# Kernel tuning notes

Measured on AMD Instinct MI355X. Metric: run time of the kernel, lower is better.

The kernel has to match this reference:

```python
import jax, jax.numpy as jnp
import numpy as np

B, C, L, H = 4, 512, 2048, 8
DH = C // H
SCALE = DH ** -0.5
EPS = 1e-5  # torch LayerNorm default


def setup_inputs() -> dict:
    key = jax.random.key(0)
    ks = jax.random.split(key, 3)
    x = jax.random.normal(ks[0], (B, C, L), dtype=jnp.float32)
    # Conv1d kernel_size=1 == per-position linear; weights ~ N(0, 1/C)
    w_qkv = jax.random.normal(ks[1], (3 * C, C), dtype=jnp.float32) / np.sqrt(C)
    b_qkv = jnp.zeros((3 * C,), dtype=jnp.float32)
    # NOTE: original uses zero_module(proj_out); random weights used here so the
    # baseline is non-trivial for kernel correctness testing.
    w_proj = jax.random.normal(ks[2], (C, C), dtype=jnp.float32) / np.sqrt(C)
    b_proj = jnp.zeros((C,), dtype=jnp.float32)
    ln_gamma = jnp.ones((C,), dtype=jnp.float32)
    ln_beta = jnp.zeros((C,), dtype=jnp.float32)
    return {"x": x, "ln_gamma": ln_gamma, "ln_beta": ln_beta,
            "w_qkv": w_qkv, "b_qkv": b_qkv, "w_proj": w_proj, "b_proj": b_proj}


def reference(x, ln_gamma, ln_beta, w_qkv, b_qkv, w_proj, b_proj):
    # ChannelNorm: LayerNorm over channel dim. Work in [B, L, C] layout.
    h = jnp.swapaxes(x, 1, 2)                      # [B, L, C]
    mu = jnp.mean(h, axis=-1, keepdims=True)
    var = jnp.mean((h - mu) ** 2, axis=-1, keepdims=True)
    hn = (h - mu) * jax.lax.rsqrt(var + EPS) * ln_gamma + ln_beta

    # QKV 1x1 conv as GEMM: [B, L, 3C]
    qkv = jnp.einsum('blc,dc->bld', hn, w_qkv) + b_qkv
    qkv = qkv.reshape(B, L, 3, H, DH)
    q, k, v = (qkv[:, :, i].transpose(0, 2, 1, 3) for i in range(3))  # [B, H, L, DH]

    # Scaled dot-product attention (full O(L^2) scores, as in source)
    w = jnp.einsum('bhqd,bhkd->bhqk', q, k) * SCALE
    w = jax.nn.softmax(w, axis=-1)
    o = jnp.einsum('bhqk,bhkd->bhqd', w, v)        # [B, H, L, DH]
    o = o.transpose(0, 2, 1, 3).reshape(B, L, C)

    # proj_out 1x1 conv + residual (dropout in eval mode = identity)
    out = jnp.einsum('blc,dc->bld', o, w_proj) + b_proj
    return jnp.swapaxes(out, 1, 2) + x             # [B, C, L]
```

## Files before the change

kernel.cpp:

```cpp
#include <hip/hip_runtime.h>
#include <hip/hip_bf16.h>

typedef __bf16 bf16;
typedef bf16 bf16x8 __attribute__((ext_vector_type(8)));
typedef bf16 bf16x4 __attribute__((ext_vector_type(4)));
typedef float f32x4 __attribute__((ext_vector_type(4)));

constexpr int B = 4, C = 512, L = 2048, H = 8, DH = 64;
constexpr int BL = B * L;
constexpr int BH = B * H;
constexpr int N_QKV = 3 * C;
constexpr float QSCALE = 0.125f * 1.44269504088896f;
constexpr float EPS = 1e-5f;

constexpr size_t SZ = (size_t)BL * C;
constexpr size_t OFF_HN    = 0;
constexpr size_t OFF_WQKV  = OFF_HN    + SZ * 2;
constexpr size_t OFF_WPROJ = OFF_WQKV  + (size_t)N_QKV * C * 2;
constexpr size_t OFF_Q     = OFF_WPROJ + (size_t)C * C * 2;
constexpr size_t OFF_K     = OFF_Q     + SZ * 2;
constexpr size_t OFF_V     = OFF_K     + SZ * 2;
constexpr size_t OFF_O     = OFF_V     + SZ * 2;
constexpr size_t OFF_STATS = OFF_O     + SZ * 2;
constexpr size_t OFF_OPART = OFF_STATS + (size_t)BL * 2 * 4;
constexpr size_t OFF_ML    = OFF_OPART + (size_t)2 * BH * L * DH * 2;

__device__ __forceinline__ bf16x8 ld8(const bf16* p) {
  return *(const bf16x8*)p;
}

__device__ __forceinline__ void gll16(const bf16* g, bf16* l) {
  __builtin_amdgcn_global_load_lds(
      (const __attribute__((address_space(1))) unsigned int*)(const void*)g,
      (__attribute__((address_space(3))) unsigned int*)(void*)l, 16, 0, 0);
}

__device__ __forceinline__ unsigned pack_bf16(float a, float b) {
  unsigned ua = __builtin_bit_cast(unsigned, a) + 0x8000u;
  unsigned ub = __builtin_bit_cast(unsigned, b) + 0x8000u;
  return __builtin_amdgcn_perm(ub, ua, 0x07060302u);
}
__device__ __forceinline__ float bf_lo(unsigned u) { return __builtin_bit_cast(float, u << 16); }
__device__ __forceinline__ float bf_hi(unsigned u) { return __builtin_bit_cast(float, u & 0xFFFF0000u); }

__global__ __launch_bounds__(256) void k_convert_w(const float* __restrict__ wqkv,
                                                   const float* __restrict__ wproj,
                                                   bf16* __restrict__ wqkv_b,
                                                   bf16* __restrict__ wproj_b) {
  int i = blockIdx.x * 256 + threadIdx.x;
  if (i < N_QKV * C) wqkv_b[i] = (bf16)wqkv[i];
  if (i < C * C)     wproj_b[i] = (bf16)wproj[i];
}

__global__ __launch_bounds__(1024) void k_ln_stats(const float* __restrict__ x,
                                                   float* __restrict__ stats) {
  int blk = blockIdx.x;
  int b = blk >> 5;
  int l0 = (blk & 31) << 6;
  int lane = threadIdx.x & 63;
  int w = threadIdx.x >> 6;
  const float* xp = x + ((size_t)b * C) * L + l0 + lane;
  float s = 0.f, ss = 0.f;
#pragma unroll
  for (int r = 0; r < 32; ++r) {
    float v = xp[(size_t)(w + r * 16) * L];
    s += v; ss += v * v;
  }
  __shared__ float sh_s[16][64];
  __shared__ float sh_q[16][64];
  sh_s[w][lane] = s; sh_q[w][lane] = ss;
  __syncthreads();
  if (threadIdx.x < 64) {
    float ts = 0.f, tq = 0.f;
#pragma unroll
    for (int i = 0; i < 16; ++i) { ts += sh_s[i][lane]; tq += sh_q[i][lane]; }
    float mu = ts * (1.0f / C);
    float var = tq * (1.0f / C) - mu * mu;
    float rstd = rsqrtf(var + EPS);
    int idx = b * L + l0 + lane;
    stats[idx * 2]     = mu;
    stats[idx * 2 + 1] = rstd;
  }
}

__global__ __launch_bounds__(256) void k_ln_norm(const float* __restrict__ x,
                                                 const float* __restrict__ stats,
                                                 const float* __restrict__ gamma,
                                                 const float* __restrict__ beta,
                                                 bf16* __restrict__ hn) {
  int blk = blockIdx.x;
  int ct = blk & 7;  blk >>= 3;
  int lt = blk & 31; int b = blk >> 5;
  int c0 = ct << 6, l0 = lt << 6;
  int lane = threadIdx.x & 63, w = threadIdx.x >> 6;
  __shared__ float tile[64][65];
  const float* xp = x + (size_t)(b * C + c0) * L + l0;
#pragma unroll
  for (int r = 0; r < 16; ++r) {
    int c = w * 16 + r;
    tile[c][lane] = xp[(size_t)c * L + lane];
  }
  __syncthreads();
  float g = gamma[c0 + lane], be = beta[c0 + lane];
  bf16* hp = hn + (size_t)(b * L + l0) * C + c0 + lane;
#pragma unroll
  for (int r = 0; r < 16; ++r) {
    int ll = w * 16 + r;
    float mu   = stats[(b * L + l0 + ll) * 2];
    float rstd = stats[(b * L + l0 + ll) * 2 + 1];
    float v = (tile[lane][ll] - mu) * rstd * g + be;
    hp[(size_t)ll * C] = (bf16)v;
  }
}

__global__ __launch_bounds__(256) void k_gemm_qkv(const bf16* __restrict__ hn,
                                                  const bf16* __restrict__ wq,
                                                  const float* __restrict__ bq,
                                                  bf16* __restrict__ qg,
                                                  bf16* __restrict__ kg,
                                                  bf16* __restrict__ vg) {
  int mt = blockIdx.x, nt = blockIdx.y;
  int m0 = mt << 7, n0 = nt << 7;
  int t = threadIdx.x, lane = t & 63, w = t >> 6;
  int mw = w >> 1, nw = w & 1;
  int q4 = lane >> 4, c16 = lane & 15;
  __shared__ __align__(16) char smem[36864];
  bf16* As = (bf16*)smem;
  bf16* Bs = (bf16*)(smem + 16384);

  int goff[4], ldsoff[4];
#pragma unroll
  for (int p = 0; p < 4; ++p) {
    int idx = (p * 4 + w) * 64 + lane;
    int row = idx >> 3, s0 = idx & 7;
    goff[p] = row * C + (s0 ^ (row & 7)) * 8;
    ldsoff[p] = (p * 4 + w) * 512;
  }

  f32x4 acc[4][4];
#pragma unroll
  for (int mi = 0; mi < 4; ++mi)
#pragma unroll
    for (int ni = 0; ni < 4; ++ni) acc[mi][ni] = (f32x4){0.f, 0.f, 0.f, 0.f};

  const bf16* ap = hn + (size_t)m0 * C;
  const bf16* bp = wq + (size_t)n0 * C;
  for (int k0 = 0; k0 < C; k0 += 64) {
    __syncthreads();
#pragma unroll
    for (int p = 0; p < 4; ++p) {
      gll16(ap + k0 + goff[p], As + ldsoff[p]);
      gll16(bp + k0 + goff[p], Bs + ldsoff[p]);
    }
    __syncthreads();
#pragma unroll
    for (int kk2 = 0; kk2 < 2; ++kk2) {
      bf16x8 af[4], bfr[4];
#pragma unroll
      for (int mi = 0; mi < 4; ++mi) {
        int row = mw * 64 + mi * 16 + c16;
        af[mi] = ld8(As + row * 64 + ((kk2 * 4 + q4) ^ (row & 7)) * 8);
      }
#pragma unroll
      for (int ni = 0; ni < 4; ++ni) {
        int row = nw * 64 + ni * 16 + c16;
        bfr[ni] = ld8(Bs + row * 64 + ((kk2 * 4 + q4) ^ (row & 7)) * 8);
      }
#pragma unroll
      for (int mi = 0; mi < 4; ++mi)
#pragma unroll
        for (int ni = 0; ni < 4; ++ni)
          acc[mi][ni] = __builtin_amdgcn_mfma_f32_16x16x32_bf16(af[mi], bfr[ni], acc[mi][ni], 0, 0, 0);
    }
  }
  __syncthreads();

  int i = nt >> 2;
  int h = ((nt & 3) << 1) + nw;
  int b = m0 >> 11;
  int l0 = (m0 & (L - 1)) + mw * 64;
  float bias[4];
#pragma unroll
  for (int ni = 0; ni < 4; ++ni) bias[ni] = bq[n0 + nw * 64 + ni * 16 + c16];
  bf16* Os = (bf16*)(smem + w * 9216);

  if (i == 2) {
#pragma unroll
    for (int mi = 0; mi < 4; ++mi)
#pragma unroll
      for (int ni = 0; ni < 4; ++ni) {
        bf16x4 pk;
#pragma unroll
        for (int r = 0; r < 4; ++r) pk[r] = (bf16)(acc[mi][ni][r] + bias[ni]);
        *(bf16x4*)&Os[(ni * 16 + c16) * 72 + mi * 16 + q4 * 4] = pk;
      }
    __syncthreads();
    const bf16* src = Os + lane * 72;
    bf16* dst = vg + ((size_t)((b * H + h) * DH + lane)) * L + l0;
#pragma unroll
    for (int s = 0; s < 8; ++s)
      *(uint4*)(dst + s * 8) = *(const uint4*)(src + s * 8);
  } else {
    float sc = (i == 0) ? QSCALE : 1.0f;
#pragma unroll
    for (int mi = 0; mi < 4; ++mi)
#pragma unroll
      for (int ni = 0; ni < 4; ++ni)
#pragma unroll
        for (int r = 0; r < 4; ++r)
          Os[(mi * 16 + q4 * 4 + r) * 72 + ni * 16 + c16] = (bf16)((acc[mi][ni][r] + bias[ni]) * sc);
    __syncthreads();
    bf16* dst0 = (i == 0) ? qg : kg;
    const bf16* src = Os + lane * 72;
    bf16* dst = dst0 + ((size_t)((b * H + h) * L + l0 + lane)) * DH;
#pragma unroll
    for (int s = 0; s < 8; ++s)
      *(uint4*)(dst + s * 8) = *(const uint4*)(src + s * 8);
  }
}

__global__ __launch_bounds__(128, 4) void k_attn(const bf16* __restrict__ qg,
                                                 const bf16* __restrict__ kg,
                                                 const bf16* __restrict__ vt,
                                                 bf16* __restrict__ opart,
                                                 float* __restrict__ lsum) {
  int blk = blockIdx.x;
  int js = blk & 1; blk >>= 1;
  int qt = blk & 31; int bh = blk >> 5;
  int t = threadIdx.x, lane = t & 63, w = t >> 6;
  int q4 = lane >> 4, c16 = lane & 15;
  __shared__ __align__(16) bf16 Ks[64][64];
  __shared__ __align__(16) bf16 Vts[64][64];
  __shared__ __align__(16) bf16 Ps[2][16][72];
  const bf16* qptr  = qg + ((size_t)bh * L + qt * 64 + w * 32) * DH;
  const bf16* kptr  = kg + (size_t)bh * L * DH;
  const bf16* vtptr = vt + (size_t)bh * DH * L;

  int ksoff[4], vsoff[4];
#pragma unroll
  for (int p = 0; p < 4; ++p) {
    int idx = (p * 2 + w) * 64 + lane;
    int r = idx >> 3, s0 = idx & 7;
    int ch = s0 ^ (r & 7);
    ksoff[p] = r * DH + ch * 8;
    vsoff[p] = r * L + ch * 8;
  }
  int sw = c16 & 7;

  bf16x8 qf[2][2];
#pragma unroll
  for (int qb = 0; qb < 2; ++qb)
#pragma unroll
    for (int kk2 = 0; kk2 < 2; ++kk2)
      qf[qb][kk2] = ld8(&qptr[(size_t)(qb * 16 + c16) * DH + kk2 * 32 + q4 * 8]);

  f32x4 o_acc[2][4];
  float l_i[2] = {0.f, 0.f};
#pragma unroll
  for (int qb = 0; qb < 2; ++qb)
#pragma unroll
    for (int db = 0; db < 4; ++db) o_acc[qb][db] = (f32x4){0.f, 0.f, 0.f, 0.f};

  for (int j0 = js * 1024; j0 < js * 1024 + 1024; j0 += 64) {
    __syncthreads();
#pragma unroll
    for (int p = 0; p < 4; ++p) {
      gll16(kptr + (size_t)j0 * DH + ksoff[p], &Ks[0][0]  + (p * 2 + w) * 512);
      gll16(vtptr + j0 + vsoff[p],             &Vts[0][0] + (p * 2 + w) * 512);
    }
    __syncthreads();

    f32x4 s[2][4];
#pragma unroll
    for (int qb = 0; qb < 2; ++qb)
#pragma unroll
      for (int jb = 0; jb < 4; ++jb) s[qb][jb] = (f32x4){0.f, 0.f, 0.f, 0.f};
#pragma unroll
    for (int kk2 = 0; kk2 < 2; ++kk2) {
      int choff = ((kk2 * 4 + q4) ^ sw) * 8;
#pragma unroll
      for (int jb = 0; jb < 4; ++jb) {
        bf16x8 kf = ld8(&Ks[0][0] + (jb * 16 + c16) * 64 + choff);
        s[0][jb] = __builtin_amdgcn_mfma_f32_16x16x32_bf16(kf, qf[0][kk2], s[0][jb], 0, 0, 0);
        s[1][jb] = __builtin_amdgcn_mfma_f32_16x16x32_bf16(kf, qf[1][kk2], s[1][jb], 0, 0, 0);
      }
    }

#pragma unroll
    for (int qb = 0; qb < 2; ++qb) {
      float rs = 0.f;
#pragma unroll
      for (int jb = 0; jb < 4; ++jb)
#pragma unroll
        for (int r = 0; r < 4; ++r) {
          float p_ = __builtin_amdgcn_exp2f(s[qb][jb][r]);
          s[qb][jb][r] = p_;
          rs += p_;
        }
      l_i[qb] += rs;
    }

    bf16x8 vf[2][4];
#pragma unroll
    for (int kk2 = 0; kk2 < 2; ++kk2) {
      int choff = ((kk2 * 4 + q4) ^ sw) * 8;
#pragma unroll
      for (int db = 0; db < 4; ++db)
        vf[kk2][db] = ld8(&Vts[0][0] + (db * 16 + c16) * 64 + choff);
    }

#pragma unroll
    for (int qb = 0; qb < 2; ++qb) {
#pragma unroll
      for (int jb = 0; jb < 4; ++jb) {
        uint2 pk;
        pk.x = pack_bf16(s[qb][jb][0], s[qb][jb][1]);
        pk.y = pack_bf16(s[qb][jb][2], s[qb][jb][3]);
        *(uint2*)&Ps[w][c16][jb * 16 + q4 * 4] = pk;
      }
#pragma unroll
      for (int kk2 = 0; kk2 < 2; ++kk2) {
        bf16x8 pf = ld8(&Ps[w][c16][kk2 * 32 + q4 * 8]);
#pragma unroll
        for (int db = 0; db < 4; ++db)
          o_acc[qb][db] = __builtin_amdgcn_mfma_f32_16x16x32_bf16(vf[kk2][db], pf, o_acc[qb][db], 0, 0, 0);
      }
    }
  }

#pragma unroll
  for (int qb = 0; qb < 2; ++qb) {
    float lf = l_i[qb];
    lf += __shfl_xor(lf, 16, 64);
    lf += __shfl_xor(lf, 32, 64);
    int q = qt * 64 + w * 32 + qb * 16 + c16;
    bf16* op = opart + (((size_t)js * BH + bh) * L + q) * DH;
#pragma unroll
    for (int db = 0; db < 4; ++db) {
      uint2 pk;
      pk.x = pack_bf16(o_acc[qb][db][0], o_acc[qb][db][1]);
      pk.y = pack_bf16(o_acc[qb][db][2], o_acc[qb][db][3]);
      *(uint2*)&op[db * 16 + q4 * 4] = pk;
    }
    if (q4 == 0) lsum[((size_t)js * BH + bh) * L + q] = lf;
  }
}

__global__ __launch_bounds__(256) void k_merge(const bf16* __restrict__ opart,
                                               const float* __restrict__ lsum,
                                               bf16* __restrict__ ob) {
  int blk = blockIdx.x;
  int qt = blk & 31, bh = blk >> 5;
  int t = threadIdx.x;
  int q = qt * 64 + (t >> 2);
  int seg = t & 3;
  float l0 = lsum[(size_t)bh * L + q];
  float l1 = lsum[((size_t)BH + bh) * L + q];
  float inv = __builtin_amdgcn_rcpf(l0 + l1);
  const uint4* p0 = (const uint4*)(opart + ((size_t)bh * L + q) * DH + seg * 16);
  const uint4* p1 = (const uint4*)(opart + (((size_t)BH + bh) * L + q) * DH + seg * 16);
  int b = bh >> 3, h = bh & 7;
  uint4* dst = (uint4*)(ob + ((size_t)b * L + q) * C + h * DH + seg * 16);
#pragma unroll
  for (int i = 0; i < 2; ++i) {
    uint4 a0 = p0[i], a1 = p1[i];
    uint4 o;
    unsigned* pa0 = (unsigned*)&a0;
    unsigned* pa1 = (unsigned*)&a1;
    unsigned* po  = (unsigned*)&o;
#pragma unroll
    for (int k = 0; k < 4; ++k) {
      float lo = (bf_lo(pa0[k]) + bf_lo(pa1[k])) * inv;
      float hi = (bf_hi(pa0[k]) + bf_hi(pa1[k])) * inv;
      po[k] = pack_bf16(lo, hi);
    }
    dst[i] = o;
  }
}

__global__ __launch_bounds__(256) void k_gemm_proj(const bf16* __restrict__ ob,
                                                   const bf16* __restrict__ wp,
                                                   const float* __restrict__ bp,
                                                   const float* __restrict__ x,
                                                   float* __restrict__ out) {
  int mt = blockIdx.x, nt = blockIdx.y;
  int m0 = mt << 6, n0 = nt << 6;
  int t = threadIdx.x;
  int lane = t & 63, w = t >> 6;
  int q4 = lane >> 4, c16 = lane & 15;
  __shared__ __align__(16) bf16 As[64][72];
  __shared__ __align__(16) bf16 Bs[64][72];
  __shared__ float Ot[64][65];
  f32x4 acc[4];
#pragma unroll
  for (int nb = 0; nb < 4; ++nb) acc[nb] = (f32x4){0.f, 0.f, 0.f, 0.f};

  for (int k0 = 0; k0 < C; k0 += 64) {
    __syncthreads();
#pragma unroll
    for (int p = 0; p < 2; ++p) {
      int idx = p * 256 + t;
      int row = idx >> 3, ch = idx & 7;
      *(bf16x8*)&As[row][ch * 8] = *(const bf16x8*)&ob[(size_t)(m0 + row) * C + k0 + ch * 8];
      *(bf16x8*)&Bs[row][ch * 8] = *(const bf16x8*)&wp[(size_t)(n0 + row) * C + k0 + ch * 8];
    }
    __syncthreads();
#pragma unroll
    for (int kk = 0; kk < 64; kk += 32) {
      bf16x8 a = ld8(&As[w * 16 + c16][kk + q4 * 8]);
#pragma unroll
      for (int nb = 0; nb < 4; ++nb) {
        bf16x8 bfr = ld8(&Bs[nb * 16 + c16][kk + q4 * 8]);
        acc[nb] = __builtin_amdgcn_mfma_f32_16x16x32_bf16(a, bfr, acc[nb], 0, 0, 0);
      }
    }
  }
  __syncthreads();
#pragma unroll
  for (int nb = 0; nb < 4; ++nb)
#pragma unroll
    for (int r = 0; r < 4; ++r)
      Ot[w * 16 + q4 * 4 + r][nb * 16 + c16] = acc[nb][r];
  __syncthreads();
  int b = m0 >> 11, l0 = m0 & (L - 1);
#pragma unroll
  for (int r = 0; r < 16; ++r) {
    int cl = w * 16 + r;
    int c = n0 + cl;
    size_t idx = (size_t)(b * C + c) * L + l0 + lane;
    out[idx] = Ot[lane][cl] + bp[c] + x[idx];
  }
}

extern "C" void kernel_launch(void* const* d_in, const int* in_sizes, int n_in,
                              void* d_out, int out_size, void* d_ws, size_t ws_size,
                              hipStream_t stream) {
  const float* x     = (const float*)d_in[0];
  const float* gamma = (const float*)d_in[1];
  const float* beta  = (const float*)d_in[2];
  const float* wqkv  = (const float*)d_in[3];
  const float* bqkv  = (const float*)d_in[4];
  const float* wproj = (const float*)d_in[5];
  const float* bproj = (const float*)d_in[6];
  float* out = (float*)d_out;
  char* ws = (char*)d_ws;
  bf16* hn  = (bf16*)(ws + OFF_HN);
  bf16* wqb = (bf16*)(ws + OFF_WQKV);
  bf16* wpb = (bf16*)(ws + OFF_WPROJ);
  bf16* qbp = (bf16*)(ws + OFF_Q);
  bf16* kbp = (bf16*)(ws + OFF_K);
  bf16* vbp = (bf16*)(ws + OFF_V);
  bf16* obp = (bf16*)(ws + OFF_O);
  float* stats = (float*)(ws + OFF_STATS);
  bf16* opart = (bf16*)(ws + OFF_OPART);
  float* lsum = (float*)(ws + OFF_ML);

  hipLaunchKernelGGL(k_convert_w, dim3((N_QKV * C + 255) / 256), dim3(256), 0, stream,
                     wqkv, wproj, wqb, wpb);
  hipLaunchKernelGGL(k_ln_stats, dim3(B * (L / 64)), dim3(1024), 0, stream, x, stats);
  hipLaunchKernelGGL(k_ln_norm, dim3(B * (L / 64) * (C / 64)), dim3(256), 0, stream,
                     x, stats, gamma, beta, hn);
  hipLaunchKernelGGL(k_gemm_qkv, dim3(BL / 128, N_QKV / 128), dim3(256), 0, stream,
                     hn, wqb, bqkv, qbp, kbp, vbp);
  hipLaunchKernelGGL(k_attn, dim3(B * H * (L / 64) * 2), dim3(128), 0, stream,
                     qbp, kbp, vbp, opart, lsum);
  hipLaunchKernelGGL(k_merge, dim3(BH * (L / 64)), dim3(256), 0, stream, opart, lsum, obp);
  hipLaunchKernelGGL(k_gemm_proj, dim3(BL / 64, C / 64), dim3(256), 0, stream,
                     obp, wpb, bproj, x, out);
}
```

Baseline: 202.0 us.

## Fuse LayerNorm passes, fold split-K merge into proj GEMM, widen attention blocks

Merges the two LayerNorm kernels into one that keeps a 512x32 tile of x in LDS, so x is read once and the stats buffer round trip goes away. Removes the separate merge kernel: the projection GEMM now reads both attention partial outputs, combines them and normalises by the summed row sums while staging its A tile. Attention blocks grow to 256 threads covering 128 queries, so each K/V tile load is shared by twice as many queries. The costs are a large LDS footprint in the LN kernel, which limits occupancy, and the merge arithmetic being repeated by every N-tile of the proj GEMM.

```diff
diff --git a/kernel.cpp b/kernel.cpp
--- a/kernel.cpp
+++ b/kernel.cpp
@@ -52,64 +52,52 @@
   if (i < C * C)     wproj_b[i] = (bf16)wproj[i];
 }
 
-__global__ __launch_bounds__(1024) void k_ln_stats(const float* __restrict__ x,
-                                                   float* __restrict__ stats) {
+__global__ __launch_bounds__(1024) void k_ln(const float* __restrict__ x,
+                                             const float* __restrict__ gamma,
+                                             const float* __restrict__ beta,
+                                             bf16* __restrict__ hn) {
   int blk = blockIdx.x;
-  int b = blk >> 5;
-  int l0 = (blk & 31) << 6;
-  int lane = threadIdx.x & 63;
-  int w = threadIdx.x >> 6;
-  const float* xp = x + ((size_t)b * C) * L + l0 + lane;
+  int b = blk >> 6;
+  int l0 = (blk & 63) << 5;
+  int t = threadIdx.x;
+  int ll = t & 31;
+  int cg = t >> 5;
+  __shared__ float tile[512][33];
+  __shared__ float sh_s[32][33];
+  __shared__ float sh_q[32][33];
+  __shared__ float mu_s[32], rs_s[32];
+  const float* xp = x + ((size_t)b * C) * L + l0;
   float s = 0.f, ss = 0.f;
 #pragma unroll
-  for (int r = 0; r < 32; ++r) {
-    float v = xp[(size_t)(w + r * 16) * L];
+  for (int r = 0; r < 16; ++r) {
+    int c = cg * 16 + r;
+    float v = xp[(size_t)c * L + ll];
+    tile[c][ll] = v;
     s += v; ss += v * v;
   }
-  __shared__ float sh_s[16][64];
-  __shared__ float sh_q[16][64];
-  sh_s[w][lane] = s; sh_q[w][lane] = ss;
+  sh_s[cg][ll] = s; sh_q[cg][ll] = ss;
   __syncthreads();
-  if (threadIdx.x < 64) {
+  if (t < 32) {
     float ts = 0.f, tq = 0.f;
 #pragma unroll
-    for (int i = 0; i < 16; ++i) { ts += sh_s[i][lane]; tq += sh_q[i][lane]; }
+    for (int i = 0; i < 32; ++i) { ts += sh_s[i][t]; tq += sh_q[i][t]; }
     float mu = ts * (1.0f / C);
     float var = tq * (1.0f / C) - mu * mu;
-    float rstd = rsqrtf(var + EPS);
-    int idx = b * L + l0 + lane;
-    stats[idx * 2]     = mu;
-    stats[idx * 2 + 1] = rstd;
-  }
-}
-
-__global__ __launch_bounds__(256) void k_ln_norm(const float* __restrict__ x,
-                                                 const float* __restrict__ stats,
-                                                 const float* __restrict__ gamma,
-                                                 const float* __restrict__ beta,
-                                                 bf16* __restrict__ hn) {
-  int blk = blockIdx.x;
-  int ct = blk & 7;  blk >>= 3;
-  int lt = blk & 31; int b = blk >> 5;
-  int c0 = ct << 6, l0 = lt << 6;
-  int lane = threadIdx.x & 63, w = threadIdx.x >> 6;
-  __shared__ float tile[64][65];
-  const float* xp = x + (size_t)(b * C + c0) * L + l0;
-#pragma unroll
-  for (int r = 0; r < 16; ++r) {
-    int c = w * 16 + r;
-    tile[c][lane] = xp[(size_t)c * L + lane];
+    mu_s[t] = mu;
+    rs_s[t] = rsqrtf(var + EPS);
   }
   __syncthreads();
-  float g = gamma[c0 + lane], be = beta[c0 + lane];
-  bf16* hp = hn + (size_t)(b * L + l0) * C + c0 + lane;
-#pragma unroll
-  for (int r = 0; r < 16; ++r) {
-    int ll = w * 16 + r;
-    float mu   = stats[(b * L + l0 + ll) * 2];
-    float rstd = stats[(b * L + l0 + ll) * 2 + 1];
-    float v = (tile[lane][ll] - mu) * rstd * g + be;
-    hp[(size_t)ll * C] = (bf16)v;
+  int c2 = (t & 255) * 2;
+  int lgrp = t >> 8;
+  float g0 = gamma[c2], g1 = gamma[c2 + 1];
+  float b0 = beta[c2],  b1 = beta[c2 + 1];
+#pragma unroll
+  for (int it = 0; it < 8; ++it) {
+    int l = lgrp * 8 + it;
+    float mu = mu_s[l], rstd = rs_s[l];
+    float v0 = (tile[c2][l]     - mu) * rstd * g0 + b0;
+    float v1 = (tile[c2 + 1][l] - mu) * rstd * g1 + b1;
+    *(unsigned*)&hn[(size_t)(b * L + l0 + l) * C + c2] = pack_bf16(v0, v1);
   }
 }
 
@@ -219,31 +207,31 @@
   }
 }
 
-__global__ __launch_bounds__(128, 4) void k_attn(const bf16* __restrict__ qg,
+__global__ __launch_bounds__(256, 4) void k_attn(const bf16* __restrict__ qg,
                                                  const bf16* __restrict__ kg,
                                                  const bf16* __restrict__ vt,
                                                  bf16* __restrict__ opart,
                                                  float* __restrict__ lsum) {
   int blk = blockIdx.x;
   int js = blk & 1; blk >>= 1;
-  int qt = blk & 31; int bh = blk >> 5;
+  int qt = blk & 15; int bh = blk >> 4;
   int t = threadIdx.x, lane = t & 63, w = t >> 6;
   int q4 = lane >> 4, c16 = lane & 15;
   __shared__ __align__(16) bf16 Ks[64][64];
   __shared__ __align__(16) bf16 Vts[64][64];
-  __shared__ __align__(16) bf16 Ps[2][16][72];
-  const bf16* qptr  = qg + ((size_t)bh * L + qt * 64 + w * 32) * DH;
+  __shared__ __align__(16) bf16 Ps[4][16][72];
+  const bf16* qptr  = qg + ((size_t)bh * L + qt * 128 + w * 32) * DH;
   const bf16* kptr  = kg + (size_t)bh * L * DH;
   const bf16* vtptr = vt + (size_t)bh * DH * L;
 
-  int ksoff[4], vsoff[4];
-#pragma unroll
-  for (int p = 0; p < 4; ++p) {
-    int idx = (p * 2 + w) * 64 + lane;
-    int r = idx >> 3, s0 = idx & 7;
-    int ch = s0 ^ (r & 7);
-    ksoff[p] = r * DH + ch * 8;
-    vsoff[p] = r * L + ch * 8;
+  int ksoff[2], vsoff[2];
+#pragma unroll
+  for (int p = 0; p < 2; ++p) {
+    int ci = p * 256 + w * 64 + lane;
+    int row = ci >> 3, s0 = ci & 7;
+    int ch = s0 ^ (row & 7);
+    ksoff[p] = row * DH + ch * 8;
+    vsoff[p] = row * L + ch * 8;
   }
   int sw = c16 & 7;
 
@@ -264,9 +252,9 @@
   for (int j0 = js * 1024; j0 < js * 1024 + 1024; j0 += 64) {
     __syncthreads();
 #pragma unroll
-    for (int p = 0; p < 4; ++p) {
-      gll16(kptr + (size_t)j0 * DH + ksoff[p], &Ks[0][0]  + (p * 2 + w) * 512);
-      gll16(vtptr + j0 + vsoff[p],             &Vts[0][0] + (p * 2 + w) * 512);
+    for (int p = 0; p < 2; ++p) {
+      gll16(kptr + (size_t)j0 * DH + ksoff[p], &Ks[0][0]  + (p * 4 + w) * 512);
+      gll16(vtptr + j0 + vsoff[p],             &Vts[0][0] + (p * 4 + w) * 512);
     }
     __syncthreads();
 
@@ -333,7 +321,7 @@
     float lf = l_i[qb];
     lf += __shfl_xor(lf, 16, 64);
     lf += __shfl_xor(lf, 32, 64);
-    int q = qt * 64 + w * 32 + qb * 16 + c16;
+    int q = qt * 128 + w * 32 + qb * 16 + c16;
     bf16* op = opart + (((size_t)js * BH + bh) * L + q) * DH;
 #pragma unroll
     for (int db = 0; db < 4; ++db) {
@@ -346,39 +334,8 @@
   }
 }
 
-__global__ __launch_bounds__(256) void k_merge(const bf16* __restrict__ opart,
-                                               const float* __restrict__ lsum,
-                                               bf16* __restrict__ ob) {
-  int blk = blockIdx.x;
-  int qt = blk & 31, bh = blk >> 5;
-  int t = threadIdx.x;
-  int q = qt * 64 + (t >> 2);
-  int seg = t & 3;
-  float l0 = lsum[(size_t)bh * L + q];
-  float l1 = lsum[((size_t)BH + bh) * L + q];
-  float inv = __builtin_amdgcn_rcpf(l0 + l1);
-  const uint4* p0 = (const uint4*)(opart + ((size_t)bh * L + q) * DH + seg * 16);
-  const uint4* p1 = (const uint4*)(opart + (((size_t)BH + bh) * L + q) * DH + seg * 16);
-  int b = bh >> 3, h = bh & 7;
-  uint4* dst = (uint4*)(ob + ((size_t)b * L + q) * C + h * DH + seg * 16);
-#pragma unroll
-  for (int i = 0; i < 2; ++i) {
-    uint4 a0 = p0[i], a1 = p1[i];
-    uint4 o;
-    unsigned* pa0 = (unsigned*)&a0;
-    unsigned* pa1 = (unsigned*)&a1;
-    unsigned* po  = (unsigned*)&o;
-#pragma unroll
-    for (int k = 0; k < 4; ++k) {
-      float lo = (bf_lo(pa0[k]) + bf_lo(pa1[k])) * inv;
-      float hi = (bf_hi(pa0[k]) + bf_hi(pa1[k])) * inv;
-      po[k] = pack_bf16(lo, hi);
-    }
-    dst[i] = o;
-  }
-}
-
-__global__ __launch_bounds__(256) void k_gemm_proj(const bf16* __restrict__ ob,
+__global__ __launch_bounds__(256) void k_gemm_proj(const bf16* __restrict__ opart,
+                                                   const float* __restrict__ lsum,
                                                    const bf16* __restrict__ wp,
                                                    const float* __restrict__ bp,
                                                    const float* __restrict__ x,
@@ -391,18 +348,41 @@
   __shared__ __align__(16) bf16 As[64][72];
   __shared__ __align__(16) bf16 Bs[64][72];
   __shared__ float Ot[64][65];
+  __shared__ float invs[64][9];
+  int b = m0 >> 11, q0 = m0 & (L - 1);
+  for (int i = t; i < 512; i += 256) {
+    int row = i >> 3, h = i & 7;
+    int bhh = b * 8 + h;
+    float l0v = lsum[(size_t)bhh * L + q0 + row];
+    float l1v = lsum[((size_t)BH + bhh) * L + q0 + row];
+    invs[row][h] = 1.0f / (l0v + l1v);
+  }
   f32x4 acc[4];
 #pragma unroll
   for (int nb = 0; nb < 4; ++nb) acc[nb] = (f32x4){0.f, 0.f, 0.f, 0.f};
 
   for (int k0 = 0; k0 < C; k0 += 64) {
     __syncthreads();
+    int h = k0 >> 6;
+    const bf16* ap0 = opart + ((size_t)(b * 8 + h) * L + q0) * 64;
+    const bf16* ap1 = opart + ((size_t)(BH + b * 8 + h) * L + q0) * 64;
 #pragma unroll
     for (int p = 0; p < 2; ++p) {
       int idx = p * 256 + t;
       int row = idx >> 3, ch = idx & 7;
-      *(bf16x8*)&As[row][ch * 8] = *(const bf16x8*)&ob[(size_t)(m0 + row) * C + k0 + ch * 8];
-      *(bf16x8*)&Bs[row][ch * 8] = *(const bf16x8*)&wp[(size_t)(n0 + row) * C + k0 + ch * 8];
+      uint4 u0 = *(const uint4*)(ap0 + (size_t)row * 64 + ch * 8);
+      uint4 u1 = *(const uint4*)(ap1 + (size_t)row * 64 + ch * 8);
+      float inv = invs[row][h];
+      unsigned* pu0 = (unsigned*)&u0;
+      unsigned* pu1 = (unsigned*)&u1;
+      uint4 m;
+      unsigned* pm = (unsigned*)&m;
+#pragma unroll
+      for (int k = 0; k < 4; ++k)
+        pm[k] = pack_bf16((bf_lo(pu0[k]) + bf_lo(pu1[k])) * inv,
+                          (bf_hi(pu0[k]) + bf_hi(pu1[k])) * inv);
+      *(uint4*)&As[row][ch * 8] = m;
+      *(bf16x8*)&Bs[row][ch * 8] = ld8(&wp[(size_t)(n0 + row) * C + k0 + ch * 8]);
     }
     __syncthreads();
 #pragma unroll
@@ -422,12 +402,11 @@
     for (int r = 0; r < 4; ++r)
       Ot[w * 16 + q4 * 4 + r][nb * 16 + c16] = acc[nb][r];
   __syncthreads();
-  int b = m0 >> 11, l0 = m0 & (L - 1);
 #pragma unroll
   for (int r = 0; r < 16; ++r) {
     int cl = w * 16 + r;
     int c = n0 + cl;
-    size_t idx = (size_t)(b * C + c) * L + l0 + lane;
+    size_t idx = (size_t)(b * C + c) * L + q0 + lane;
     out[idx] = Ot[lane][cl] + bp[c] + x[idx];
   }
 }
@@ -450,21 +429,17 @@
   bf16* qbp = (bf16*)(ws + OFF_Q);
   bf16* kbp = (bf16*)(ws + OFF_K);
   bf16* vbp = (bf16*)(ws + OFF_V);
-  bf16* obp = (bf16*)(ws + OFF_O);
-  float* stats = (float*)(ws + OFF_STATS);
   bf16* opart = (bf16*)(ws + OFF_OPART);
   float* lsum = (float*)(ws + OFF_ML);
 
   hipLaunchKernelGGL(k_convert_w, dim3((N_QKV * C + 255) / 256), dim3(256), 0, stream,
                      wqkv, wproj, wqb, wpb);
-  hipLaunchKernelGGL(k_ln_stats, dim3(B * (L / 64)), dim3(1024), 0, stream, x, stats);
-  hipLaunchKernelGGL(k_ln_norm, dim3(B * (L / 64) * (C / 64)), dim3(256), 0, stream,
-                     x, stats, gamma, beta, hn);
+  hipLaunchKernelGGL(k_ln, dim3(B * (L / 32)), dim3(1024), 0, stream,
+                     x, gamma, beta, hn);
   hipLaunchKernelGGL(k_gemm_qkv, dim3(BL / 128, N_QKV / 128), dim3(256), 0, stream,
                      hn, wqb, bqkv, qbp, kbp, vbp);
-  hipLaunchKernelGGL(k_attn, dim3(B * H * (L / 64) * 2), dim3(128), 0, stream,
+  hipLaunchKernelGGL(k_attn, dim3(B * H * (L / 128) * 2), dim3(256), 0, stream,
                      qbp, kbp, vbp, opart, lsum);
-  hipLaunchKernelGGL(k_merge, dim3(BH * (L / 64)), dim3(256), 0, stream, opart, lsum, obp);
   hipLaunchKernelGGL(k_gemm_proj, dim3(BL / 64, C / 64), dim3(256), 0, stream,
-                     obp, wpb, bproj, x, out);
-}
+                     opart, lsum, wpb, bproj, x, out);
+}
```

Result: faster. 174.3 us (-13.7%).
